# Performance work log

Measured on AMD Instinct MI355X. Metric: run time of the kernel, lower is better.

The kernel has to match this reference:

```python
import math
import jax, jax.numpy as jnp
import numpy as np

B, T, D, V, L, H = 2, 1024, 768, 32768, 4, 12
HD = D // H
STD = 0.02


def layer_norm(x, w, b):
    mu = x.mean(-1, keepdims=True)
    var = ((x - mu) ** 2).mean(-1, keepdims=True)
    return (x - mu) * jax.lax.rsqrt(var + 1e-5) * w + b


def new_gelu(x):
    c = math.sqrt(2.0 / math.pi)
    return 0.5 * x * (1.0 + jnp.tanh(c * (x + 0.044715 * x ** 3)))


def setup_inputs() -> dict:
    key = jax.random.key(0)
    ks = jax.random.split(key, 10)
    idx = jax.random.randint(ks[0], (B, T), 0, V)
    age = jax.random.uniform(ks[1], (B, T), dtype=jnp.float32) * 36500.0  # days
    wte = jax.random.normal(ks[2], (V, D), jnp.float32) * STD  # tied with lm_head
    wae_w = jax.random.normal(ks[3], (D, D), jnp.float32) * STD  # AgeEncoding linear (no bias)
    proj_std = STD / math.sqrt(2 * L)
    return {
        'idx': idx,
        'age': age,
        'wte': wte,
        'wae_w': wae_w,
        'ln1_w': jnp.ones((L, D), jnp.float32),
        'ln1_b': jnp.zeros((L, D), jnp.float32),
        'attn_w': jax.random.normal(ks[4], (L, 3 * D, D), jnp.float32) * STD,
        'attn_b': jnp.zeros((L, 3 * D), jnp.float32),
        'proj_w': jax.random.normal(ks[5], (L, D, D), jnp.float32) * proj_std,
        'proj_b': jnp.zeros((L, D), jnp.float32),
        'ln2_w': jnp.ones((L, D), jnp.float32),
        'ln2_b': jnp.zeros((L, D), jnp.float32),
        'fc_w': jax.random.normal(ks[6], (L, 4 * D, D), jnp.float32) * STD,
        'fc_b': jnp.zeros((L, 4 * D), jnp.float32),
        'fc2_w': jax.random.normal(ks[7], (L, D, 4 * D), jnp.float32) * proj_std,
        'fc2_b': jnp.zeros((L, D), jnp.float32),
        'lnf_w': jnp.ones((D,), jnp.float32),
        'lnf_b': jnp.zeros((D,), jnp.float32),
    }


def _forward(idx, age, wte, wae_w, ln1_w, ln1_b, attn_w, attn_b, proj_w, proj_b,
             ln2_w, ln2_b, fc_w, fc_b, fc2_w, fc2_b, lnf_w, lnf_b):
    # token embedding (tied with lm_head)
    tok = wte[idx]  # [B,T,D]
    # age encoding: interleaved sin/cos of age/365.25 * div_term, then linear
    div = jnp.exp(jnp.arange(0, D, 2).astype(jnp.float32) * (-math.log(10000.0) / D))  # [D/2]
    ang = (age[..., None] / 365.25) * div  # [B,T,D/2]
    y = jnp.zeros((B, T, D), tok.dtype)
    y = y.at[..., 0::2].set(jnp.sin(ang)).at[..., 1::2].set(jnp.cos(ang))
    x = tok + y @ wae_w.T  # token_drop identity at dropout 0 (scaled by 1-0)

    # attention mask: valid-token outer product, causal, plus self-attn for pad tokens
    valid = idx > 0
    tril = jnp.tril(jnp.ones((T, T), bool))
    mask = valid[:, None, None, :] & valid[:, None, :, None] & tril
    mask = (mask | ((~valid)[:, None, None, :] & jnp.eye(T, dtype=bool))) & tril  # [B,1,T,T]

    scale = 1.0 / math.sqrt(HD)

    def block(x, p):
        l1w, l1b, aw, ab, pw, pb, l2w, l2b, fw, fb, f2w, f2b = p
        h = layer_norm(x, l1w, l1b)
        qkv = h @ aw.T + ab
        q, k, v = jnp.split(qkv, 3, axis=-1)
        q = q.reshape(B, T, H, HD).transpose(0, 2, 1, 3)  # [B,H,T,HD]
        k = k.reshape(B, T, H, HD).transpose(0, 2, 1, 3)
        v = v.reshape(B, T, H, HD).transpose(0, 2, 1, 3)
        att = jnp.einsum('bhqd,bhkd->bhqk', q, k) * scale
        att = jnp.where(mask, att, -jnp.inf)
        att = jax.nn.softmax(att, axis=-1)
        yv = jnp.einsum('bhqk,bhkd->bhqd', att, v)
        yv = yv.transpose(0, 2, 1, 3).reshape(B, T, D)
        x = x + yv @ pw.T + pb
        h2 = layer_norm(x, l2w, l2b)
        x = x + new_gelu(h2 @ fw.T + fb) @ f2w.T + f2b
        return x, att

    x, att = jax.lax.scan(block, x, (ln1_w, ln1_b, attn_w, attn_b, proj_w, proj_b,
                                     ln2_w, ln2_b, fc_w, fc_b, fc2_w, fc2_b))
    x = layer_norm(x, lnf_w, lnf_b)
    logits = x @ wte.T  # tied lm_head
    return logits


def reference(idx, age, wte, wae_w, ln1_w, ln1_b, attn_w, attn_b, proj_w, proj_b,
              ln2_w, ln2_b, fc_w, fc_b, fc2_w, fc2_b, lnf_w, lnf_b):
    return _forward(idx, age, wte, wae_w, ln1_w, ln1_b, attn_w, attn_b, proj_w, proj_b,
                    ln2_w, ln2_b, fc_w, fc_b, fc2_w, fc2_b, lnf_w, lnf_b)
```

## Files before the change

### kernel.cpp

```cpp
#include <hip/hip_runtime.h>

typedef unsigned short u16;
typedef __bf16 bf16x8 __attribute__((ext_vector_type(8)));
typedef float f32x4 __attribute__((ext_vector_type(4)));

__device__ __forceinline__ u16 f2bf(float f) {
    union { float f; unsigned int u; } c; c.f = f;
    unsigned int u = c.u;
    unsigned int r = (u + 0x7FFFu + ((u >> 16) & 1u)) >> 16;
    return (u16)r;
}

__device__ __forceinline__ float gelu_f(float v) {
    const float c = 0.7978845608028654f;
    float t = tanhf(c * (v + 0.044715f * v * v * v));
    return 0.5f * v * (1.0f + t);
}

typedef const __attribute__((address_space(1))) unsigned int* as1_u32p;
typedef __attribute__((address_space(3))) unsigned int* as3_u32p;
__device__ __forceinline__ void gload16(const void* g, void* l) {
    __builtin_amdgcn_global_load_lds((as1_u32p)g, (as3_u32p)l, 16, 0, 0);
}

template <int N> __device__ __forceinline__ void wait_vmcnt() {
    if constexpr (N == 0)      asm volatile("s_waitcnt vmcnt(0)" ::: "memory");
    else if constexpr (N == 3) asm volatile("s_waitcnt vmcnt(3)" ::: "memory");
    else if constexpr (N == 4) asm volatile("s_waitcnt vmcnt(4)" ::: "memory");
    else if constexpr (N == 6) asm volatile("s_waitcnt vmcnt(6)" ::: "memory");
    else if constexpr (N == 8) asm volatile("s_waitcnt vmcnt(8)" ::: "memory");
}

__global__ __launch_bounds__(256) void cvt_kernel(
    const float* __restrict__ src, u16* __restrict__ dst, int n4)
{
    int i = blockIdx.x * 256 + threadIdx.x;
    int stride = gridDim.x * 256;
    for (; i < n4; i += stride) {
        float4 f = reinterpret_cast<const float4*>(src)[i];
        union { u16 h[4]; uint2 u; } cv;
        cv.h[0] = f2bf(f.x); cv.h[1] = f2bf(f.y);
        cv.h[2] = f2bf(f.z); cv.h[3] = f2bf(f.w);
        reinterpret_cast<uint2*>(dst)[i] = cv.u;
    }
}

__global__ __launch_bounds__(256) void embed_kernel(
    const int* __restrict__ idx, const float* __restrict__ age,
    const float* __restrict__ wte, float* __restrict__ x, u16* __restrict__ y)
{
    int t = blockIdx.x;
    int tid = threadIdx.x;
    int tok = idx[t];
    float a = age[t] * (1.0f / 365.25f);
    const float kc = -9.210340371976184f / 768.0f;
#pragma unroll
    for (int j = 0; j < 3; j++) {
        int d = tid + j * 256;
        x[(size_t)t * 768 + d] = wte[(size_t)tok * 768 + d];
        int twoi = d & ~1;
        float dv = __expf(kc * (float)twoi);
        float ang = a * dv;
        float val = (d & 1) ? __cosf(ang) : __sinf(ang);
        y[(size_t)t * 768 + d] = f2bf(val);
    }
}

__global__ __launch_bounds__(256) void ln_kernel(
    const float* __restrict__ x, const float* __restrict__ w,
    const float* __restrict__ b, u16* __restrict__ out)
{
    int row = blockIdx.x;
    int tid = threadIdx.x;
    int l = tid & 63, wv = tid >> 6;
    const float* xr = x + (size_t)row * 768;
    float v[3], s = 0.f, ss = 0.f;
#pragma unroll
    for (int j = 0; j < 3; j++) { v[j] = xr[tid + j * 256]; s += v[j]; ss += v[j] * v[j]; }
#pragma unroll
    for (int d = 1; d < 64; d <<= 1) { s += __shfl_xor(s, d); ss += __shfl_xor(ss, d); }
    __shared__ float ps[4], pss[4];
    if (l == 0) { ps[wv] = s; pss[wv] = ss; }
    __syncthreads();
    s = ps[0] + ps[1] + ps[2] + ps[3];
    ss = pss[0] + pss[1] + pss[2] + pss[3];
    float mu = s * (1.0f / 768.0f);
    float var = ss * (1.0f / 768.0f) - mu * mu;
    float rstd = rsqrtf(var + 1e-5f);
#pragma unroll
    for (int j = 0; j < 3; j++) {
        int d = tid + j * 256;
        out[(size_t)row * 768 + d] = f2bf((v[j] - mu) * rstd * w[d] + b[d]);
    }
}

enum { EPI_BF16 = 0, EPI_BF16_GELU = 1, EPI_F32_RESID = 2, EPI_F32 = 3 };

template <int EPI, int BM, int NWM>
__global__ __launch_bounds__(256) void gemm_p3_kernel(
    const u16* __restrict__ A, const u16* __restrict__ B,
    const float* __restrict__ bias, const float* resid, void* out,
    int N, int K, int mtiles, int nwg8)
{
    constexpr int NWN = 4 / NWM;
    constexpr int MI  = (BM / NWM) / 16;
    constexpr int NI  = (128 / NWN) / 16;
    constexpr int ASHOTS = (BM * 4) / 256;
    constexpr int LPS = ASHOTS + 2;
    __shared__ u16 As[4][BM][32];
    __shared__ u16 Bs[4][128][32];
    int tid = threadIdx.x;
    int l = tid & 63, w = tid >> 6;
    int lw = l & 15, lg = l >> 4;
    int bid = blockIdx.x;
    int wg = (bid & 7) * nwg8 + (bid >> 3);
    int mt = wg % mtiles, nt = wg / mtiles;
    int row0 = mt * BM, col0 = nt * 128;
    int wm = w % NWM, wn = w / NWM;
    int mbase = wm * (BM / NWM), nbase = wn * (128 / NWN);

    f32x4 acc[MI][NI] = {};
    const int ntiles = K >> 5;

    auto stage = [&](int nb, int kk) {
        u16* asb = &As[nb][0][0];
        u16* bsb = &Bs[nb][0][0];
#pragma unroll
        for (int s = 0; s < ASHOTS; s++) {
            int c = s * 256 + tid;
            int r = c >> 2, q = (c & 3) * 8;
            gload16(A + (size_t)(row0 + r) * K + kk + q, asb + r * 32 + q);
        }
#pragma unroll
        for (int s = 0; s < 2; s++) {
            int c = s * 256 + tid;
            int r = c >> 2, q = (c & 3) * 8;
            gload16(B + (size_t)(col0 + r) * K + kk + q, bsb + r * 32 + q);
        }
    };

    stage(0, 0);
    stage(1, 32);
    stage(2, 64);
    wait_vmcnt<2 * LPS>();
    __builtin_amdgcn_s_barrier();

    for (int t = 0; t < ntiles; ++t) {
        int cur = t & 3;
        bf16x8 af[MI], bfr[NI];
#pragma unroll
        for (int mi = 0; mi < MI; mi++)
            af[mi] = *reinterpret_cast<const bf16x8*>(&As[cur][mbase + mi * 16 + lw][lg * 8]);
#pragma unroll
        for (int ni = 0; ni < NI; ni++)
            bfr[ni] = *reinterpret_cast<const bf16x8*>(&Bs[cur][nbase + ni * 16 + lw][lg * 8]);
        if (t + 3 < ntiles) stage((t + 3) & 3, (t + 3) << 5);
        __builtin_amdgcn_s_setprio(1);
#pragma unroll
        for (int mi = 0; mi < MI; mi++)
#pragma unroll
            for (int ni = 0; ni < NI; ni++)
                acc[mi][ni] = __builtin_amdgcn_mfma_f32_16x16x32_bf16(af[mi], bfr[ni], acc[mi][ni], 0, 0, 0);
        __builtin_amdgcn_s_setprio(0);
        int rem = ntiles - 1 - t;
        if (rem >= 3)      wait_vmcnt<2 * LPS>();
        else if (rem == 2) wait_vmcnt<LPS>();
        else if (rem == 1) wait_vmcnt<0>();
        __builtin_amdgcn_s_barrier();
    }

#pragma unroll
    for (int mi = 0; mi < MI; mi++) {
#pragma unroll
        for (int ni = 0; ni < NI; ni++) {
            int colc = col0 + nbase + ni * 16 + lw;
            float bv = bias ? bias[colc] : 0.0f;
#pragma unroll
            for (int j = 0; j < 4; j++) {
                int row = row0 + mbase + mi * 16 + lg * 4 + j;
                size_t off = (size_t)row * N + colc;
                float v = acc[mi][ni][j] + bv;
                if constexpr (EPI == EPI_BF16) {
                    ((u16*)out)[off] = f2bf(v);
                } else if constexpr (EPI == EPI_BF16_GELU) {
                    ((u16*)out)[off] = f2bf(gelu_f(v));
                } else if constexpr (EPI == EPI_F32_RESID) {
                    ((float*)out)[off] = v + resid[off];
                } else {
                    ((float*)out)[off] = v;
                }
            }
        }
    }
}

template <int EPI>
__global__ __launch_bounds__(256) void gemm_kernel(
    const u16* __restrict__ A, const float* __restrict__ Bw,
    const float* __restrict__ bias, const float* resid, void* out,
    int N, int K)
{
    constexpr int M = 2048;
    __shared__ u16 As[128][40];
    __shared__ u16 Bs[128][40];
    int tid = threadIdx.x;
    int l = tid & 63, w = tid >> 6;
    int lw = l & 15, lg = l >> 4;
    int mtiles = M / 128;
    int mt = blockIdx.x % mtiles, nt = blockIdx.x / mtiles;
    int row0 = mt * 128, col0 = nt * 128;
    int mbase = (w & 1) * 64, nbase = (w >> 1) * 64;
    f32x4 acc[4][4] = {};

    for (int kk = 0; kk < K; kk += 32) {
        int c = tid;
#pragma unroll
        for (int i = 0; i < 2; i++, c += 256) {
            int r = c >> 2, q = c & 3;
            uint4 u = *reinterpret_cast<const uint4*>(A + (size_t)(row0 + r) * K + kk + q * 8);
            *reinterpret_cast<uint4*>(&As[r][q * 8]) = u;
        }
        int c2 = tid;
#pragma unroll
        for (int i = 0; i < 4; i++, c2 += 256) {
            int r = c2 >> 3, q = c2 & 7;
            const float4 f = *reinterpret_cast<const float4*>(Bw + (size_t)(col0 + r) * K + kk + q * 4);
            union { u16 h[4]; uint2 u; } cv;
            cv.h[0] = f2bf(f.x); cv.h[1] = f2bf(f.y); cv.h[2] = f2bf(f.z); cv.h[3] = f2bf(f.w);
            *reinterpret_cast<uint2*>(&Bs[r][q * 4]) = cv.u;
        }
        __syncthreads();
        bf16x8 af[4], bfr[4];
#pragma unroll
        for (int mi = 0; mi < 4; mi++)
            af[mi] = *reinterpret_cast<const bf16x8*>(&As[mbase + mi * 16 + lw][lg * 8]);
#pragma unroll
        for (int ni = 0; ni < 4; ni++)
            bfr[ni] = *reinterpret_cast<const bf16x8*>(&Bs[nbase + ni * 16 + lw][lg * 8]);
#pragma unroll
        for (int mi = 0; mi < 4; mi++)
#pragma unroll
            for (int ni = 0; ni < 4; ni++)
                acc[mi][ni] = __builtin_amdgcn_mfma_f32_16x16x32_bf16(af[mi], bfr[ni], acc[mi][ni], 0, 0, 0);
        __syncthreads();
    }

#pragma unroll
    for (int mi = 0; mi < 4; mi++) {
#pragma unroll
        for (int ni = 0; ni < 4; ni++) {
            int colc = col0 + nbase + ni * 16 + lw;
            float bv = bias ? bias[colc] : 0.0f;
#pragma unroll
            for (int j = 0; j < 4; j++) {
                int row = row0 + mbase + mi * 16 + lg * 4 + j;
                size_t off = (size_t)row * N + colc;
                float v = acc[mi][ni][j] + bv;
                if constexpr (EPI == EPI_BF16) {
                    ((u16*)out)[off] = f2bf(v);
                } else if constexpr (EPI == EPI_BF16_GELU) {
                    ((u16*)out)[off] = f2bf(gelu_f(v));
                } else if constexpr (EPI == EPI_F32_RESID) {
                    ((float*)out)[off] = v + resid[off];
                } else {
                    ((float*)out)[off] = v;
                }
            }
        }
    }
}

__global__ __launch_bounds__(256) void attn_kernel(
    const u16* __restrict__ qkv, const int* __restrict__ idx, u16* __restrict__ yv)
{
    __shared__ u16 Kt[32][72];
    __shared__ u16 Vt[64][40];
    __shared__ u16 Pb[4][16][40];
    __shared__ int kval[32];

    int tid = threadIdx.x, l = tid & 63, w = tid >> 6;
    int lw = l & 15, lg = l >> 4;
    int bid = blockIdx.x;
    int qb = bid & 15;
    int h = (bid >> 4) % 12;
    int b = bid / (16 * 12);
    const size_t base = (size_t)b * 1024;

    int qrow = qb * 64 + w * 16 + lw;
    const u16* qp = qkv + (base + qrow) * 2304 + h * 64;
    bf16x8 aq0 = *reinterpret_cast<const bf16x8*>(qp + lg * 8);
    bf16x8 aq1 = *reinterpret_cast<const bf16x8*>(qp + 32 + lg * 8);

    int rowj[4], vq[4];
#pragma unroll
    for (int j = 0; j < 4; j++) {
        rowj[j] = qb * 64 + w * 16 + lg * 4 + j;
        vq[j] = idx[base + rowj[j]] > 0;
    }
    float m[4], lsum[4];
    f32x4 O[4] = {};
#pragma unroll
    for (int j = 0; j < 4; j++) { m[j] = -__builtin_inff(); lsum[j] = 0.0f; }

    int kvend = qb * 64 + 64;
    for (int kv0 = 0; kv0 < kvend; kv0 += 32) {
        {
            int r = tid >> 3, cc = tid & 7;
            const u16* kp = qkv + (base + kv0 + r) * 2304 + 768 + h * 64 + cc * 8;
            uint4 ku = *reinterpret_cast<const uint4*>(kp);
            *reinterpret_cast<uint4*>(&Kt[r][cc * 8]) = ku;
            const u16* vp = qkv + (base + kv0 + r) * 2304 + 1536 + h * 64 + cc * 8;
            union { uint4 u; u16 h8[8]; } vu;
            vu.u = *reinterpret_cast<const uint4*>(vp);
#pragma unroll
            for (int j2 = 0; j2 < 8; j2++) Vt[cc * 8 + j2][r] = vu.h8[j2];
            if (tid < 32) kval[tid] = idx[base + kv0 + tid] > 0;
        }
        __syncthreads();

        f32x4 S[2];
#pragma unroll
        for (int g = 0; g < 2; g++) {
            bf16x8 bk0 = *reinterpret_cast<const bf16x8*>(&Kt[g * 16 + lw][lg * 8]);
            bf16x8 bk1 = *reinterpret_cast<const bf16x8*>(&Kt[g * 16 + lw][32 + lg * 8]);
            f32x4 t = {};
            t = __builtin_amdgcn_mfma_f32_16x16x32_bf16(aq0, bk0, t, 0, 0, 0);
            t = __builtin_amdgcn_mfma_f32_16x16x32_bf16(aq1, bk1, t, 0, 0, 0);
            S[g] = t;
        }
        float p[2][4];
#pragma unroll
        for (int j = 0; j < 4; j++) {
            float sv0, sv1;
#pragma unroll
            for (int g = 0; g < 2; g++) {
                int kcol = kv0 + g * 16 + lw;
                float s = S[g][j] * 0.125f;
                bool keep = (kcol <= rowj[j]) &&
                            ((vq[j] && kval[g * 16 + lw]) || (kcol == rowj[j]));
                s = keep ? s : -__builtin_inff();
                if (g) sv1 = s; else sv0 = s;
            }
            float mx = fmaxf(sv0, sv1);
            mx = fmaxf(mx, __shfl_xor(mx, 1));
            mx = fmaxf(mx, __shfl_xor(mx, 2));
            mx = fmaxf(mx, __shfl_xor(mx, 4));
            mx = fmaxf(mx, __shfl_xor(mx, 8));
            float mn = fmaxf(m[j], mx);
            float mclamp = fmaxf(mn, -1e30f);
            float scale = __expf(m[j] - mclamp);
            float p0 = __expf(sv0 - mclamp);
            float p1 = __expf(sv1 - mclamp);
            float rs = p0 + p1;
            rs += __shfl_xor(rs, 1); rs += __shfl_xor(rs, 2);
            rs += __shfl_xor(rs, 4); rs += __shfl_xor(rs, 8);
            lsum[j] = lsum[j] * scale + rs;
            m[j] = mn;
#pragma unroll
            for (int ni = 0; ni < 4; ni++) O[ni][j] *= scale;
            p[0][j] = p0; p[1][j] = p1;
        }
#pragma unroll
        for (int g = 0; g < 2; g++)
#pragma unroll
            for (int j = 0; j < 4; j++)
                Pb[w][lg * 4 + j][g * 16 + lw] = f2bf(p[g][j]);
        bf16x8 ap = *reinterpret_cast<const bf16x8*>(&Pb[w][lw][lg * 8]);
#pragma unroll
        for (int ni = 0; ni < 4; ni++) {
            bf16x8 bv = *reinterpret_cast<const bf16x8*>(&Vt[ni * 16 + lw][lg * 8]);
            O[ni] = __builtin_amdgcn_mfma_f32_16x16x32_bf16(ap, bv, O[ni], 0, 0, 0);
        }
        __syncthreads();
    }

#pragma unroll
    for (int j = 0; j < 4; j++) {
        float inv = 1.0f / lsum[j];
#pragma unroll
        for (int ni = 0; ni < 4; ni++) {
            float v = O[ni][j] * inv;
            yv[(base + rowj[j]) * 768 + h * 64 + ni * 16 + lw] = f2bf(v);
        }
    }
}

static void launch_gemm_db(int epi, const u16* A, const u16* B, const float* bias,
                           const float* resid, void* out, int N, int K, hipStream_t s)
{
    dim3 blk(256);
    if (N == 768) {
        constexpr int BM = 64, NWM = 1;
        int mtiles = 2048 / BM;
        int nwg = mtiles * (N / 128);
        dim3 grid(nwg);
        int nwg8 = nwg / 8;
        switch (epi) {
            case EPI_BF16:      gemm_p3_kernel<EPI_BF16, BM, NWM><<<grid, blk, 0, s>>>(A, B, bias, resid, out, N, K, mtiles, nwg8); break;
            case EPI_BF16_GELU: gemm_p3_kernel<EPI_BF16_GELU, BM, NWM><<<grid, blk, 0, s>>>(A, B, bias, resid, out, N, K, mtiles, nwg8); break;
            case EPI_F32_RESID: gemm_p3_kernel<EPI_F32_RESID, BM, NWM><<<grid, blk, 0, s>>>(A, B, bias, resid, out, N, K, mtiles, nwg8); break;
            default:            gemm_p3_kernel<EPI_F32, BM, NWM><<<grid, blk, 0, s>>>(A, B, bias, resid, out, N, K, mtiles, nwg8); break;
        }
    } else {
        constexpr int BM = 128, NWM = 2;
        int mtiles = 2048 / BM;
        int nwg = mtiles * (N / 128);
        dim3 grid(nwg);
        int nwg8 = nwg / 8;
        switch (epi) {
            case EPI_BF16:      gemm_p3_kernel<EPI_BF16, BM, NWM><<<grid, blk, 0, s>>>(A, B, bias, resid, out, N, K, mtiles, nwg8); break;
            case EPI_BF16_GELU: gemm_p3_kernel<EPI_BF16_GELU, BM, NWM><<<grid, blk, 0, s>>>(A, B, bias, resid, out, N, K, mtiles, nwg8); break;
            case EPI_F32_RESID: gemm_p3_kernel<EPI_F32_RESID, BM, NWM><<<grid, blk, 0, s>>>(A, B, bias, resid, out, N, K, mtiles, nwg8); break;
            default:            gemm_p3_kernel<EPI_F32, BM, NWM><<<grid, blk, 0, s>>>(A, B, bias, resid, out, N, K, mtiles, nwg8); break;
        }
    }
}

static void launch_gemm_f32w(int epi, const u16* A, const float* Bw, const float* bias,
                             const float* resid, void* out, int N, int K, hipStream_t s)
{
    dim3 grid((2048 / 128) * (N / 128)), blk(256);
    switch (epi) {
        case EPI_BF16:      gemm_kernel<EPI_BF16><<<grid, blk, 0, s>>>(A, Bw, bias, resid, out, N, K); break;
        case EPI_BF16_GELU: gemm_kernel<EPI_BF16_GELU><<<grid, blk, 0, s>>>(A, Bw, bias, resid, out, N, K); break;
        case EPI_F32_RESID: gemm_kernel<EPI_F32_RESID><<<grid, blk, 0, s>>>(A, Bw, bias, resid, out, N, K); break;
        default:            gemm_kernel<EPI_F32><<<grid, blk, 0, s>>>(A, Bw, bias, resid, out, N, K); break;
    }
}

static void cvt(const float* src, u16* dst, size_t n, hipStream_t s) {
    int n4 = (int)(n / 4);
    int blocks = (n4 + 255) / 256;
    if (blocks > 2048) blocks = 2048;
    cvt_kernel<<<blocks, 256, 0, s>>>(src, dst, n4);
}

extern "C" void kernel_launch(void* const* d_in, const int* in_sizes, int n_in,
                              void* d_out, int out_size, void* d_ws, size_t ws_size,
                              hipStream_t stream)
{
    (void)in_sizes; (void)n_in; (void)out_size;
    const int*   idx    = (const int*)  d_in[0];
    const float* age    = (const float*)d_in[1];
    const float* wte    = (const float*)d_in[2];
    const float* wae_w  = (const float*)d_in[3];
    const float* ln1_w  = (const float*)d_in[4];
    const float* ln1_b  = (const float*)d_in[5];
    const float* attn_w = (const float*)d_in[6];
    const float* attn_b = (const float*)d_in[7];
    const float* proj_w = (const float*)d_in[8];
    const float* proj_b = (const float*)d_in[9];
    const float* ln2_w  = (const float*)d_in[10];
    const float* ln2_b  = (const float*)d_in[11];
    const float* fc_w   = (const float*)d_in[12];
    const float* fc_b   = (const float*)d_in[13];
    const float* fc2_w  = (const float*)d_in[14];
    const float* fc2_b  = (const float*)d_in[15];
    const float* lnf_w  = (const float*)d_in[16];
    const float* lnf_b  = (const float*)d_in[17];

    char* ws = (char*)d_ws;
    size_t off = 0;
    float* x   = (float*)(ws + off); off += (size_t)2048 * 768 * 4;
    u16* hb    = (u16*)(ws + off);   off += (size_t)2048 * 768 * 2;
    u16* qkvb  = (u16*)(ws + off);   off += (size_t)2048 * 2304 * 2;
    u16* yvb   = (u16*)(ws + off);   off += (size_t)2048 * 768 * 2;
    u16* a1b   = (u16*)(ws + off);   off += (size_t)2048 * 3072 * 2;
    u16* yage  = (u16*)(ws + off);   off += (size_t)2048 * 768 * 2;
    u16* wte_b  = (u16*)(ws + off);  off += (size_t)32768 * 768 * 2;
    u16* attn_wb= (u16*)(ws + off);  off += (size_t)4 * 2304 * 768 * 2;
    u16* proj_wb= (u16*)(ws + off);  off += (size_t)4 * 768 * 768 * 2;
    u16* fc_wb  = (u16*)(ws + off);  off += (size_t)4 * 3072 * 768 * 2;
    u16* fc2_wb = (u16*)(ws + off);  off += (size_t)4 * 768 * 3072 * 2;
    u16* wae_wb = (u16*)(ws + off);  off += (size_t)768 * 768 * 2;
    const size_t NEED = off;

    if (ws_size >= NEED) {
        cvt(wte,    wte_b,   (size_t)32768 * 768, stream);
        cvt(attn_w, attn_wb, (size_t)4 * 2304 * 768, stream);
        cvt(proj_w, proj_wb, (size_t)4 * 768 * 768, stream);
        cvt(fc_w,   fc_wb,   (size_t)4 * 3072 * 768, stream);
        cvt(fc2_w,  fc2_wb,  (size_t)4 * 768 * 3072, stream);
        cvt(wae_w,  wae_wb,  (size_t)768 * 768, stream);

        embed_kernel<<<2048, 256, 0, stream>>>(idx, age, wte, x, yage);
        launch_gemm_db(EPI_F32_RESID, yage, wae_wb, nullptr, x, x, 768, 768, stream);

        for (int li = 0; li < 4; li++) {
            ln_kernel<<<2048, 256, 0, stream>>>(x, ln1_w + li * 768, ln1_b + li * 768, hb);
            launch_gemm_db(EPI_BF16, hb, attn_wb + (size_t)li * 2304 * 768, attn_b + li * 2304,
                           nullptr, qkvb, 2304, 768, stream);
            attn_kernel<<<2 * 12 * 16, 256, 0, stream>>>(qkvb, idx, yvb);
            launch_gemm_db(EPI_F32_RESID, yvb, proj_wb + (size_t)li * 768 * 768, proj_b + li * 768,
                           x, x, 768, 768, stream);
            ln_kernel<<<2048, 256, 0, stream>>>(x, ln2_w + li * 768, ln2_b + li * 768, hb);
            launch_gemm_db(EPI_BF16_GELU, hb, fc_wb + (size_t)li * 3072 * 768, fc_b + li * 3072,
                           nullptr, a1b, 3072, 768, stream);
            launch_gemm_db(EPI_F32_RESID, a1b, fc2_wb + (size_t)li * 768 * 3072, fc2_b + li * 768,
                           x, x, 768, 3072, stream);
        }

        ln_kernel<<<2048, 256, 0, stream>>>(x, lnf_w, lnf_b, hb);
        launch_gemm_db(EPI_F32, hb, wte_b, nullptr, nullptr, d_out, 32768, 768, stream);
    } else {
        embed_kernel<<<2048, 256, 0, stream>>>(idx, age, wte, x, yage);
        launch_gemm_f32w(EPI_F32_RESID, yage, wae_w, nullptr, x, x, 768, 768, stream);
        for (int li = 0; li < 4; li++) {
            ln_kernel<<<2048, 256, 0, stream>>>(x, ln1_w + li * 768, ln1_b + li * 768, hb);
            launch_gemm_f32w(EPI_BF16, hb, attn_w + (size_t)li * 2304 * 768, attn_b + li * 2304,
                             nullptr, qkvb, 2304, 768, stream);
            attn_kernel<<<2 * 12 * 16, 256, 0, stream>>>(qkvb, idx, yvb);
            launch_gemm_f32w(EPI_F32_RESID, yvb, proj_w + (size_t)li * 768 * 768, proj_b + li * 768,
                             x, x, 768, 768, stream);
            ln_kernel<<<2048, 256, 0, stream>>>(x, ln2_w + li * 768, ln2_b + li * 768, hb);
            launch_gemm_f32w(EPI_BF16_GELU, hb, fc_w + (size_t)li * 3072 * 768, fc_b + li * 3072,
                             nullptr, a1b, 3072, 768, stream);
            launch_gemm_f32w(EPI_F32_RESID, a1b, fc2_w + (size_t)li * 768 * 3072, fc2_b + li * 768,
                             x, x, 768, 3072, stream);
        }
        ln_kernel<<<2048, 256, 0, stream>>>(x, lnf_w, lnf_b, hb);
        launch_gemm_f32w(EPI_F32, hb, wte, nullptr, nullptr, d_out, 32768, 768, stream);
    }
}
```

Before: 1.552 ms.

## Switch GEMM to 3-stage LDS pipeline with explicit ds_read and hoisted addressing

```diff
diff --git a/kernel.cpp b/kernel.cpp
--- a/kernel.cpp
+++ b/kernel.cpp
@@ -19,8 +19,16 @@
 
 typedef const __attribute__((address_space(1))) unsigned int* as1_u32p;
 typedef __attribute__((address_space(3))) unsigned int* as3_u32p;
+typedef const __attribute__((address_space(3))) u16* as3_cu16p;
 __device__ __forceinline__ void gload16(const void* g, void* l) {
     __builtin_amdgcn_global_load_lds((as1_u32p)g, (as3_u32p)l, 16, 0, 0);
+}
+
+__device__ __forceinline__ bf16x8 ds_read_frag(const u16* p) {
+    bf16x8 r;
+    as3_cu16p lp = (as3_cu16p)p;
+    asm volatile("ds_read_b128 %0, %1" : "=v"(r) : "v"(lp));
+    return r;
 }
 
 template <int N> __device__ __forceinline__ void wait_vmcnt() {
@@ -97,7 +105,7 @@
 enum { EPI_BF16 = 0, EPI_BF16_GELU = 1, EPI_F32_RESID = 2, EPI_F32 = 3 };
 
 template <int EPI, int BM, int NWM>
-__global__ __launch_bounds__(256) void gemm_p3_kernel(
+__global__ __launch_bounds__(256) void gemm_p2_kernel(
     const u16* __restrict__ A, const u16* __restrict__ B,
     const float* __restrict__ bias, const float* resid, void* out,
     int N, int K, int mtiles, int nwg8)
@@ -107,8 +115,8 @@
     constexpr int NI  = (128 / NWN) / 16;
     constexpr int ASHOTS = (BM * 4) / 256;
     constexpr int LPS = ASHOTS + 2;
-    __shared__ u16 As[4][BM][32];
-    __shared__ u16 Bs[4][128][32];
+    __shared__ u16 As[3][BM][32];
+    __shared__ u16 Bs[3][128][32];
     int tid = threadIdx.x;
     int l = tid & 63, w = tid >> 6;
     int lw = l & 15, lg = l >> 4;
@@ -119,6 +127,11 @@
     int wm = w % NWM, wn = w / NWM;
     int mbase = wm * (BM / NWM), nbase = wn * (128 / NWN);
 
+    const u16* ga = A + (size_t)(row0 + (tid >> 2)) * K + (tid & 3) * 8;
+    const u16* gb = B + (size_t)(col0 + (tid >> 2)) * K + (tid & 3) * 8;
+    const size_t k64 = (size_t)64 * K;
+    int dofs = tid * 8;
+
     f32x4 acc[MI][NI] = {};
     const int ntiles = K >> 5;
 
@@ -126,35 +139,31 @@
         u16* asb = &As[nb][0][0];
         u16* bsb = &Bs[nb][0][0];
 #pragma unroll
-        for (int s = 0; s < ASHOTS; s++) {
-            int c = s * 256 + tid;
-            int r = c >> 2, q = (c & 3) * 8;
-            gload16(A + (size_t)(row0 + r) * K + kk + q, asb + r * 32 + q);
-        }
-#pragma unroll
-        for (int s = 0; s < 2; s++) {
-            int c = s * 256 + tid;
-            int r = c >> 2, q = (c & 3) * 8;
-            gload16(B + (size_t)(col0 + r) * K + kk + q, bsb + r * 32 + q);
-        }
+        for (int s = 0; s < ASHOTS; s++)
+            gload16(ga + s * k64 + kk, asb + s * 2048 + dofs);
+#pragma unroll
+        for (int s = 0; s < 2; s++)
+            gload16(gb + s * k64 + kk, bsb + s * 2048 + dofs);
     };
 
     stage(0, 0);
     stage(1, 32);
-    stage(2, 64);
-    wait_vmcnt<2 * LPS>();
+    wait_vmcnt<LPS>();
     __builtin_amdgcn_s_barrier();
 
+    int cur = 0;
     for (int t = 0; t < ntiles; ++t) {
-        int cur = t & 3;
+        int prv = cur == 0 ? 2 : cur - 1;
+        if (t + 2 < ntiles) stage(prv, (t + 2) << 5);
         bf16x8 af[MI], bfr[NI];
 #pragma unroll
         for (int mi = 0; mi < MI; mi++)
-            af[mi] = *reinterpret_cast<const bf16x8*>(&As[cur][mbase + mi * 16 + lw][lg * 8]);
+            af[mi] = ds_read_frag(&As[cur][mbase + mi * 16 + lw][lg * 8]);
 #pragma unroll
         for (int ni = 0; ni < NI; ni++)
-            bfr[ni] = *reinterpret_cast<const bf16x8*>(&Bs[cur][nbase + ni * 16 + lw][lg * 8]);
-        if (t + 3 < ntiles) stage((t + 3) & 3, (t + 3) << 5);
+            bfr[ni] = ds_read_frag(&Bs[cur][nbase + ni * 16 + lw][lg * 8]);
+        asm volatile("s_waitcnt lgkmcnt(0)" ::: "memory");
+        __builtin_amdgcn_sched_barrier(0);
         __builtin_amdgcn_s_setprio(1);
 #pragma unroll
         for (int mi = 0; mi < MI; mi++)
@@ -162,11 +171,10 @@
             for (int ni = 0; ni < NI; ni++)
                 acc[mi][ni] = __builtin_amdgcn_mfma_f32_16x16x32_bf16(af[mi], bfr[ni], acc[mi][ni], 0, 0, 0);
         __builtin_amdgcn_s_setprio(0);
-        int rem = ntiles - 1 - t;
-        if (rem >= 3)      wait_vmcnt<2 * LPS>();
-        else if (rem == 2) wait_vmcnt<LPS>();
-        else if (rem == 1) wait_vmcnt<0>();
+        if (t + 2 < ntiles)      wait_vmcnt<LPS>();
+        else if (t + 1 < ntiles) wait_vmcnt<0>();
         __builtin_amdgcn_s_barrier();
+        cur = cur == 2 ? 0 : cur + 1;
     }
 
 #pragma unroll
@@ -396,10 +404,10 @@
         dim3 grid(nwg);
         int nwg8 = nwg / 8;
         switch (epi) {
-            case EPI_BF16:      gemm_p3_kernel<EPI_BF16, BM, NWM><<<grid, blk, 0, s>>>(A, B, bias, resid, out, N, K, mtiles, nwg8); break;
-            case EPI_BF16_GELU: gemm_p3_kernel<EPI_BF16_GELU, BM, NWM><<<grid, blk, 0, s>>>(A, B, bias, resid, out, N, K, mtiles, nwg8); break;
-            case EPI_F32_RESID: gemm_p3_kernel<EPI_F32_RESID, BM, NWM><<<grid, blk, 0, s>>>(A, B, bias, resid, out, N, K, mtiles, nwg8); break;
-            default:            gemm_p3_kernel<EPI_F32, BM, NWM><<<grid, blk, 0, s>>>(A, B, bias, resid, out, N, K, mtiles, nwg8); break;
+            case EPI_BF16:      gemm_p2_kernel<EPI_BF16, BM, NWM><<<grid, blk, 0, s>>>(A, B, bias, resid, out, N, K, mtiles, nwg8); break;
+            case EPI_BF16_GELU: gemm_p2_kernel<EPI_BF16_GELU, BM, NWM><<<grid, blk, 0, s>>>(A, B, bias, resid, out, N, K, mtiles, nwg8); break;
+            case EPI_F32_RESID: gemm_p2_kernel<EPI_F32_RESID, BM, NWM><<<grid, blk, 0, s>>>(A, B, bias, resid, out, N, K, mtiles, nwg8); break;
+            default:            gemm_p2_kernel<EPI_F32, BM, NWM><<<grid, blk, 0, s>>>(A, B, bias, resid, out, N, K, mtiles, nwg8); break;
         }
     } else {
         constexpr int BM = 128, NWM = 2;
@@ -408,10 +416,10 @@
         dim3 grid(nwg);
         int nwg8 = nwg / 8;
         switch (epi) {
-            case EPI_BF16:      gemm_p3_kernel<EPI_BF16, BM, NWM><<<grid, blk, 0, s>>>(A, B, bias, resid, out, N, K, mtiles, nwg8); break;
-            case EPI_BF16_GELU: gemm_p3_kernel<EPI_BF16_GELU, BM, NWM><<<grid, blk, 0, s>>>(A, B, bias, resid, out, N, K, mtiles, nwg8); break;
-            case EPI_F32_RESID: gemm_p3_kernel<EPI_F32_RESID, BM, NWM><<<grid, blk, 0, s>>>(A, B, bias, resid, out, N, K, mtiles, nwg8); break;
-            default:            gemm_p3_kernel<EPI_F32, BM, NWM><<<grid, blk, 0, s>>>(A, B, bias, resid, out, N, K, mtiles, nwg8); break;
+            case EPI_BF16:      gemm_p2_kernel<EPI_BF16, BM, NWM><<<grid, blk, 0, s>>>(A, B, bias, resid, out, N, K, mtiles, nwg8); break;
+            case EPI_BF16_GELU: gemm_p2_kernel<EPI_BF16_GELU, BM, NWM><<<grid, blk, 0, s>>>(A, B, bias, resid, out, N, K, mtiles, nwg8); break;
+            case EPI_F32_RESID: gemm_p2_kernel<EPI_F32_RESID, BM, NWM><<<grid, blk, 0, s>>>(A, B, bias, resid, out, N, K, mtiles, nwg8); break;
+            default:            gemm_p2_kernel<EPI_F32, BM, NWM><<<grid, blk, 0, s>>>(A, B, bias, resid, out, N, K, mtiles, nwg8); break;
         }
     }
 }
```

After: 1.476 ms. 1.05x faster.
